# Kernel tuning notes

Measured on AMD Instinct MI355X. Metric: run time of the kernel, lower is better.

The kernel has to match this reference:

```python
import jax, jax.numpy as jnp
import numpy as np

NEG_INF = -1e9  # torch code uses masked_fill with -1e9, not -inf


def setup_inputs() -> dict:
    key = jax.random.key(0)
    ks = jax.random.split(key, 6)
    B, S, WL, D1, D2, OUT = 32, 128, 20, 300, 300, 300
    sequence = jax.random.normal(ks[0], (B, S, WL, D1), dtype=jnp.float32)
    vector = jax.random.normal(ks[1], (B, S, D2), dtype=jnp.float32)
    char_masks = jax.random.randint(ks[2], (B, S, WL), 0, 2, dtype=jnp.int32)
    W = jax.random.normal(ks[3], (OUT, D1 + D2), dtype=jnp.float32) * (1.0 / np.sqrt(D1 + D2))
    b = jax.random.normal(ks[4], (OUT,), dtype=jnp.float32) * 0.01
    v = jax.random.uniform(ks[5], (OUT,), dtype=jnp.float32, minval=-0.01, maxval=0.01)
    return {"sequence": sequence, "vector": vector, "char_masks": char_masks,
            "W": W, "b": b, "v": v}


def reference(sequence, vector, char_masks, W, b, v):
    # sequence: (B,S,WL,D1); vector: (B,S,D2); char_masks: (B,S,WL)
    D1 = sequence.shape[-1]
    # Linear on concat([sequence, vector_expanded]) == split matmul (avoids
    # materializing the (B,S,WL,D1+D2) concat):
    Ws, Wv = W[:, :D1], W[:, D1:]
    lin = (jnp.einsum('bswd,od->bswo', sequence, Ws)
           + jnp.einsum('bsd,od->bso', vector, Wv)[:, :, None, :]
           + b)                       # (B,S,WL,OUT)
    score = jnp.einsum('bswo,o->bsw', jnp.tanh(lin), v)  # (B,S,WL)
    score = jnp.where(char_masks == 0, NEG_INF, score)
    alphas = jax.nn.softmax(score, axis=2)               # over word_len
    weighted = jnp.einsum('bsw,bswd->bsd', alphas, sequence)  # (B,S,D1)
    return weighted
```

## Files before the change

kernel.cpp:

```cpp
#include <hip/hip_runtime.h>
#include <math.h>

#define NEG_INF -1000000000.0f

#define WL_  20
#define D1_  300
#define D2_  300
#define OUT_ 300
#define BS_  4096
#define PPB  4
#define NBLK (BS_ / PPB)
#define BM   80
#define KS   10
#define FR   512

typedef __attribute__((ext_vector_type(8))) short bf16x8;
typedef __attribute__((ext_vector_type(8))) short short8v;
typedef __attribute__((ext_vector_type(4))) float f32x4;
typedef __attribute__((ext_vector_type(4))) unsigned int uint4v;

__device__ short g_Bpk[KS * 20 * FR];
__device__ short g_Vpk[256 * KS * FR];
__device__ short g_Wvpk[KS * 20 * FR];
__device__ float g_vlin[(size_t)BS_ * 320];

__device__ inline short f2bf(float f) {
    unsigned u = __float_as_uint(f);
    u += 0x7FFFu + ((u >> 16) & 1u);
    return (short)(u >> 16);
}
__device__ inline float bf2f(short s) {
    return __uint_as_float(((unsigned)(unsigned short)s) << 16);
}

__device__ inline void pack_store(short* Am, int s, int lane, float4 fa, float4 fb) {
    unsigned u0 = __float_as_uint(fa.x) + 0x8000u;
    unsigned u1 = __float_as_uint(fa.y) + 0x8000u;
    unsigned u2 = __float_as_uint(fa.z) + 0x8000u;
    unsigned u3 = __float_as_uint(fa.w) + 0x8000u;
    unsigned u4 = __float_as_uint(fb.x) + 0x8000u;
    unsigned u5 = __float_as_uint(fb.y) + 0x8000u;
    unsigned u6 = __float_as_uint(fb.z) + 0x8000u;
    unsigned u7 = __float_as_uint(fb.w) + 0x8000u;
    uint4v w;
    w.x = __builtin_amdgcn_perm(u1, u0, 0x07060302u);
    w.y = __builtin_amdgcn_perm(u3, u2, 0x07060302u);
    w.z = __builtin_amdgcn_perm(u5, u4, 0x07060302u);
    w.w = __builtin_amdgcn_perm(u7, u6, 0x07060302u);
    *(uint4v*)(Am + ((size_t)s * 64 + lane) * 8) = w;
}

#define GV (256 * KS * 64)
#define GB (KS * 20 * 64)
#define GT (GV + GB + GB)

__global__ __launch_bounds__(256) void prep_small(
    const float* __restrict__ vec, const float* __restrict__ W,
    const float* __restrict__ bias,
    short* Bpk, short* Vpk, short* Wvpk)
{
    if (!Bpk) { Bpk = g_Bpk; Vpk = g_Vpk; Wvpk = g_Wvpk; }
    const int id = blockIdx.x * 256 + threadIdx.x;
    if (id >= GT) return;
    short8v o8 = {0, 0, 0, 0, 0, 0, 0, 0};
    if (id < GV) {
        const int lane = id & 63, g = id >> 6;
        const int q = lane >> 4, l15 = lane & 15;
        const int ks = g % KS, mtile = g / KS;
        const int row = mtile * 16 + l15;
        const int k0 = ks * 32 + q * 8;
        const float* s = vec + (size_t)row * D2_ + k0;
        #pragma unroll
        for (int e = 0; e < 8; ++e) {
            const int k = k0 + e;
            if (k < D2_) o8[e] = f2bf(s[e]);
            else if (k == 319) o8[e] = (short)0x3F80;
        }
        *(short8v*)(Vpk + (size_t)id * 8) = o8;
    } else if (id < GV + GB) {
        const int id3 = id - GV;
        const int lane = id3 & 63, g = id3 >> 6;
        const int q = lane >> 4, l15 = lane & 15;
        const int ks = g / 20, tile = g % 20;
        const int o = tile * 16 + l15, k0 = ks * 32 + q * 8;
        if (o < OUT_) {
            #pragma unroll
            for (int e = 0; e < 8; ++e) {
                const int k = k0 + e;
                if (k < D1_) o8[e] = f2bf(W[(size_t)o * (D1_ + D2_) + k]);
            }
        }
        *(short8v*)(Bpk + (size_t)id3 * 8) = o8;
    } else {
        const int id4 = id - GV - GB;
        const int lane = id4 & 63, g = id4 >> 6;
        const int q = lane >> 4, l15 = lane & 15;
        const int ks = g / 20, tile = g % 20;
        const int o = tile * 16 + l15, k0 = ks * 32 + q * 8;
        if (o < OUT_) {
            #pragma unroll
            for (int e = 0; e < 8; ++e) {
                const int k = k0 + e;
                if (k < D2_)        o8[e] = f2bf(W[(size_t)o * (D1_ + D2_) + D1_ + k]);
                else if (k == 319)  o8[e] = f2bf(bias[o]);
            }
        }
        *(short8v*)(Wvpk + (size_t)id4 * 8) = o8;
    }
}

__global__ __launch_bounds__(256) void vlin_kernel(
    const short* Vpk, const short* Wvpk, float* vlin)
{
    if (!vlin) { Vpk = g_Vpk; Wvpk = g_Wvpk; vlin = g_vlin; }
    const int mtile = blockIdx.x;
    const int tid  = threadIdx.x;
    const int lane = tid & 63;
    const int wv   = tid >> 6;
    const int q = lane >> 4, l15 = lane & 15;
    f32x4 acc[5];
    #pragma unroll
    for (int j = 0; j < 5; ++j) acc[j] = {0.f, 0.f, 0.f, 0.f};
    const short* pa = Vpk + (size_t)mtile * KS * FR + lane * 8;
    const short* pb = Wvpk + (size_t)(wv * 5) * FR + lane * 8;
    #pragma unroll
    for (int ks = 0; ks < KS; ++ks) {
        const bf16x8 a = *(const bf16x8*)pa; pa += FR;
        #pragma unroll
        for (int j = 0; j < 5; ++j) {
            const bf16x8 b = *(const bf16x8*)(pb + j * FR);
            acc[j] = __builtin_amdgcn_mfma_f32_16x16x32_bf16(a, b, acc[j], 0, 0, 0);
        }
        pb += 20 * FR;
    }
    const int row0 = mtile * 16 + q * 4;
    #pragma unroll
    for (int j = 0; j < 5; ++j)
        #pragma unroll
        for (int r = 0; r < 4; ++r)
            vlin[(size_t)(row0 + r) * 320 + (wv * 5 + j) * 16 + l15] = acc[j][r];
}

__global__ __launch_bounds__(256, 3) void attn_fused(
    const float* __restrict__ seq,
    const int*   __restrict__ masks,
    const float* __restrict__ vvec,
    const short* Bpk,
    const float* vlinbuf,
    float*       __restrict__ out)
{
    if (!Bpk) { Bpk = g_Bpk; vlinbuf = g_vlin; }

    __shared__ short Am[5 * KS * FR];
    __shared__ float sp[4][BM];
    __shared__ float alpha_lds[BM];

    const int tid  = threadIdx.x;
    const int lane = tid & 63;
    const int wv   = tid >> 6;
    const int q    = lane >> 4;
    const int l15  = lane & 15;
    const int blk  = blockIdx.x;

    {
        const float* sbase = seq + (size_t)blk * BM * D1_;
        float4 ra[13], rb[13];
        #pragma unroll
        for (int it = 0; it < 13; ++it) {
            const int s = wv + it * 4;
            float4 fa = {0.f, 0.f, 0.f, 0.f}, fb = {0.f, 0.f, 0.f, 0.f};
            if (s < 50) {
                const int tile = s / KS, ks = s % KS;
                const int row = tile * 16 + l15;
                const int k0 = ks * 32 + q * 8;
                const float* p = sbase + (size_t)row * D1_ + k0;
                if (k0 < 296) { fa = *(const float4*)p; fb = *(const float4*)(p + 4); }
                else if (k0 == 296) { fa = *(const float4*)p; }
            }
            ra[it] = fa; rb[it] = fb;
        }
        #pragma unroll
        for (int it = 0; it < 13; ++it) {
            const int s = wv + it * 4;
            if (s < 50) pack_store(Am, s, lane, ra[it], rb[it]);
        }
    }

    float vj[5];
    #pragma unroll
    for (int j = 0; j < 5; ++j) {
        const int col = wv * 80 + j * 16 + l15;
        vj[j] = (col < OUT_) ? vvec[col] : 0.f;
    }
    float vlp[4][5];
    #pragma unroll
    for (int p = 0; p < 4; ++p)
        #pragma unroll
        for (int j = 0; j < 5; ++j)
            vlp[p][j] = vlinbuf[(size_t)(blk * PPB + p) * 320 + wv * 80 + j * 16 + l15];
    __syncthreads();

    f32x4 acc[5][5];
    #pragma unroll
    for (int i = 0; i < 5; ++i)
        #pragma unroll
        for (int j = 0; j < 5; ++j) acc[i][j] = {0.f, 0.f, 0.f, 0.f};

    const short* pb[5];
    #pragma unroll
    for (int j = 0; j < 5; ++j)
        pb[j] = Bpk + (size_t)(wv * 5 + j) * FR + lane * 8;

    #pragma unroll
    for (int ks = 0; ks < KS; ++ks) {
        bf16x8 a[5], b[5];
        #pragma unroll
        for (int i = 0; i < 5; ++i)
            a[i] = *(const bf16x8*)(Am + (((size_t)i * KS + ks) * 64 + lane) * 8);
        #pragma unroll
        for (int j = 0; j < 5; ++j)
            b[j] = *(const bf16x8*)(pb[j] + (size_t)ks * 20 * FR);
        #pragma unroll
        for (int i = 0; i < 5; ++i)
            #pragma unroll
            for (int j = 0; j < 5; ++j)
                acc[i][j] = __builtin_amdgcn_mfma_f32_16x16x32_bf16(a[i], b[j], acc[i][j], 0, 0, 0);
    }

    #pragma unroll
    for (int i = 0; i < 5; ++i) {
        const int pLo = (16 * i) / 20;
        const int pHi = (16 * i + 15) / 20;
        #pragma unroll
        for (int r = 0; r < 4; ++r) {
            const int row = i * 16 + q * 4 + r;
            const bool hi = (row >= 20 * pHi);
            float s = 0.f;
            #pragma unroll
            for (int j = 0; j < 5; ++j) {
                const float vlv = (pLo == pHi) ? vlp[pLo][j]
                                               : (hi ? vlp[pHi][j] : vlp[pLo][j]);
                const float x = acc[i][j][r] + vlv;
                const float e = __expf(2.f * x);
                s += (1.f - 2.f / (e + 1.f)) * vj[j];
            }
            s += __shfl_xor(s, 1, 64);
            s += __shfl_xor(s, 2, 64);
            s += __shfl_xor(s, 4, 64);
            s += __shfl_xor(s, 8, 64);
            if (l15 == 0) sp[wv][row] = s;
        }
    }
    __syncthreads();

    if (tid < 128) {
        const int p = tid >> 5;
        const int w = tid & 31;
        float s;
        if (w < WL_) {
            const int row = p * WL_ + w;
            const float sc = sp[0][row] + sp[1][row] + sp[2][row] + sp[3][row];
            const int mk = masks[(size_t)(blk * PPB + p) * WL_ + w];
            s = (mk == 0) ? NEG_INF : sc;
        } else {
            s = -INFINITY;
        }
        float m = s;
        #pragma unroll
        for (int off = 16; off; off >>= 1)
            m = fmaxf(m, __shfl_xor(m, off, 32));
        const float e = __expf(s - m);
        float sum = e;
        #pragma unroll
        for (int off = 16; off; off >>= 1)
            sum += __shfl_xor(sum, off, 32);
        if (w < WL_) alpha_lds[p * WL_ + w] = e / sum;
    }
    __syncthreads();

    if (tid < PPB * 38) {
        const int p = tid / 38, ch = tid % 38;
        const int ks2 = ch >> 2, q2 = ch & 3;
        const int wst = ch % WL_;
        float o8[8] = {0.f, 0.f, 0.f, 0.f, 0.f, 0.f, 0.f, 0.f};
        #pragma unroll
        for (int wi = 0; wi < WL_; ++wi) {
            int w = wst + wi; if (w >= WL_) w -= WL_;
            const int row = p * WL_ + w;
            const int tl = row >> 4, l = row & 15;
            const bf16x8 s8 = *(const bf16x8*)(Am + (((size_t)tl * KS + ks2) * 64 + q2 * 16 + l) * 8);
            const float a = alpha_lds[row];
            #pragma unroll
            for (int e2 = 0; e2 < 8; ++e2) o8[e2] += a * bf2f(s8[e2]);
        }
        const int d0 = ch * 8, gp = blk * PPB + p;
        float* dst = out + (size_t)gp * OUT_ + d0;
        if (d0 + 8 <= OUT_) {
            *(float4*)dst       = {o8[0], o8[1], o8[2], o8[3]};
            *(float4*)(dst + 4) = {o8[4], o8[5], o8[6], o8[7]};
        } else {
            *(float4*)dst = {o8[0], o8[1], o8[2], o8[3]};
        }
    }
}

extern "C" void kernel_launch(void* const* d_in, const int* in_sizes, int n_in,
                              void* d_out, int out_size, void* d_ws, size_t ws_size,
                              hipStream_t stream) {
    const float* seq   = (const float*)d_in[0];
    const float* vec   = (const float*)d_in[1];
    const int*   masks = (const int*)d_in[2];
    const float* W     = (const float*)d_in[3];
    const float* b     = (const float*)d_in[4];
    const float* v     = (const float*)d_in[5];
    float* out = (float*)d_out;

    constexpr size_t SZ_B = sizeof(short) * (size_t)KS * 20 * FR;
    constexpr size_t SZ_V = sizeof(short) * (size_t)256 * KS * FR;
    constexpr size_t SZ_L = sizeof(float) * (size_t)BS_ * 320;
    constexpr size_t NEED = SZ_B * 2 + SZ_V + SZ_L;
    short *Bpk = nullptr, *Wvpk = nullptr, *Vpk = nullptr;
    float *vlin = nullptr;
    if (d_ws && ws_size >= NEED) {
        char* p = (char*)d_ws;
        Bpk  = (short*)p; p += SZ_B;
        Wvpk = (short*)p; p += SZ_B;
        Vpk  = (short*)p; p += SZ_V;
        vlin = (float*)p;
    }

    prep_small<<<(GT + 255) / 256, 256, 0, stream>>>(vec, W, b, Bpk, Vpk, Wvpk);
    vlin_kernel<<<256, 256, 0, stream>>>(Vpk, Wvpk, vlin);
    attn_fused<<<NBLK, 256, 0, stream>>>(seq, masks, v, Bpk, vlin, out);
}
```

Baseline: 212.0 us.

## Fuse vector projection GEMM into attention kernel, drop vlin pass

Removes the separate vlin kernel and its packed-vector buffer. Each attention block now computes the vector-side projection (plus bias) for its 4 positions with MFMA, using only 4 of 16 rows, and broadcasts the results via shuffles. This cuts one kernel launch and the global round-trip of the vlin buffer. In exchange it wastes MFMA rows, adds per-block latency before the main GEMM, and lowers the occupancy hint from 3 to 2 blocks per CU.

After: 211.0 us. No clear change (-0.5%).

```diff
diff --git a/kernel.cpp b/kernel.cpp
--- a/kernel.cpp
+++ b/kernel.cpp
@@ -20,9 +20,7 @@
 typedef __attribute__((ext_vector_type(4))) unsigned int uint4v;
 
 __device__ short g_Bpk[KS * 20 * FR];
-__device__ short g_Vpk[256 * KS * FR];
 __device__ short g_Wvpk[KS * 20 * FR];
-__device__ float g_vlin[(size_t)BS_ * 320];
 
 __device__ inline short f2bf(float f) {
     unsigned u = __float_as_uint(f);
@@ -50,36 +48,19 @@
     *(uint4v*)(Am + ((size_t)s * 64 + lane) * 8) = w;
 }
 
-#define GV (256 * KS * 64)
 #define GB (KS * 20 * 64)
-#define GT (GV + GB + GB)
+#define GT2 (GB + GB)
 
 __global__ __launch_bounds__(256) void prep_small(
-    const float* __restrict__ vec, const float* __restrict__ W,
-    const float* __restrict__ bias,
-    short* Bpk, short* Vpk, short* Wvpk)
+    const float* __restrict__ W, const float* __restrict__ bias,
+    short* Bpk, short* Wvpk)
 {
-    if (!Bpk) { Bpk = g_Bpk; Vpk = g_Vpk; Wvpk = g_Wvpk; }
+    if (!Bpk) { Bpk = g_Bpk; Wvpk = g_Wvpk; }
     const int id = blockIdx.x * 256 + threadIdx.x;
-    if (id >= GT) return;
+    if (id >= GT2) return;
     short8v o8 = {0, 0, 0, 0, 0, 0, 0, 0};
-    if (id < GV) {
+    if (id < GB) {
         const int lane = id & 63, g = id >> 6;
-        const int q = lane >> 4, l15 = lane & 15;
-        const int ks = g % KS, mtile = g / KS;
-        const int row = mtile * 16 + l15;
-        const int k0 = ks * 32 + q * 8;
-        const float* s = vec + (size_t)row * D2_ + k0;
-        #pragma unroll
-        for (int e = 0; e < 8; ++e) {
-            const int k = k0 + e;
-            if (k < D2_) o8[e] = f2bf(s[e]);
-            else if (k == 319) o8[e] = (short)0x3F80;
-        }
-        *(short8v*)(Vpk + (size_t)id * 8) = o8;
-    } else if (id < GV + GB) {
-        const int id3 = id - GV;
-        const int lane = id3 & 63, g = id3 >> 6;
         const int q = lane >> 4, l15 = lane & 15;
         const int ks = g / 20, tile = g % 20;
         const int o = tile * 16 + l15, k0 = ks * 32 + q * 8;
@@ -90,9 +71,9 @@
                 if (k < D1_) o8[e] = f2bf(W[(size_t)o * (D1_ + D2_) + k]);
             }
         }
-        *(short8v*)(Bpk + (size_t)id3 * 8) = o8;
+        *(short8v*)(Bpk + (size_t)id * 8) = o8;
     } else {
-        const int id4 = id - GV - GB;
+        const int id4 = id - GB;
         const int lane = id4 & 63, g = id4 >> 6;
         const int q = lane >> 4, l15 = lane & 15;
         const int ks = g / 20, tile = g % 20;
@@ -109,47 +90,15 @@
     }
 }
 
-__global__ __launch_bounds__(256) void vlin_kernel(
-    const short* Vpk, const short* Wvpk, float* vlin)
-{
-    if (!vlin) { Vpk = g_Vpk; Wvpk = g_Wvpk; vlin = g_vlin; }
-    const int mtile = blockIdx.x;
-    const int tid  = threadIdx.x;
-    const int lane = tid & 63;
-    const int wv   = tid >> 6;
-    const int q = lane >> 4, l15 = lane & 15;
-    f32x4 acc[5];
-    #pragma unroll
-    for (int j = 0; j < 5; ++j) acc[j] = {0.f, 0.f, 0.f, 0.f};
-    const short* pa = Vpk + (size_t)mtile * KS * FR + lane * 8;
-    const short* pb = Wvpk + (size_t)(wv * 5) * FR + lane * 8;
-    #pragma unroll
-    for (int ks = 0; ks < KS; ++ks) {
-        const bf16x8 a = *(const bf16x8*)pa; pa += FR;
-        #pragma unroll
-        for (int j = 0; j < 5; ++j) {
-            const bf16x8 b = *(const bf16x8*)(pb + j * FR);
-            acc[j] = __builtin_amdgcn_mfma_f32_16x16x32_bf16(a, b, acc[j], 0, 0, 0);
-        }
-        pb += 20 * FR;
-    }
-    const int row0 = mtile * 16 + q * 4;
-    #pragma unroll
-    for (int j = 0; j < 5; ++j)
-        #pragma unroll
-        for (int r = 0; r < 4; ++r)
-            vlin[(size_t)(row0 + r) * 320 + (wv * 5 + j) * 16 + l15] = acc[j][r];
-}
-
-__global__ __launch_bounds__(256, 3) void attn_fused(
+__global__ __launch_bounds__(256, 2) void attn_fused(
     const float* __restrict__ seq,
+    const float* __restrict__ vec,
     const int*   __restrict__ masks,
     const float* __restrict__ vvec,
-    const short* Bpk,
-    const float* vlinbuf,
+    const short* Bpk, const short* Wvpk,
     float*       __restrict__ out)
 {
-    if (!Bpk) { Bpk = g_Bpk; vlinbuf = g_vlin; }
+    if (!Bpk) { Bpk = g_Bpk; Wvpk = g_Wvpk; }
 
     __shared__ short Am[5 * KS * FR];
     __shared__ float sp[4][BM];
@@ -192,12 +141,40 @@
         const int col = wv * 80 + j * 16 + l15;
         vj[j] = (col < OUT_) ? vvec[col] : 0.f;
     }
+
+    f32x4 vacc[5];
+    #pragma unroll
+    for (int j = 0; j < 5; ++j) vacc[j] = {0.f, 0.f, 0.f, 0.f};
+    {
+        const short* pwb = Wvpk + (size_t)(wv * 5) * FR + lane * 8;
+        const float* vp = vec + (size_t)(blk * PPB + (l15 & 3)) * D2_;
+        #pragma unroll
+        for (int ks = 0; ks < KS; ++ks) {
+            const int k0 = ks * 32 + q * 8;
+            short8v av = {0, 0, 0, 0, 0, 0, 0, 0};
+            if (l15 < PPB) {
+                #pragma unroll
+                for (int e = 0; e < 8; ++e) {
+                    const int k = k0 + e;
+                    if (k < D2_)       av[e] = f2bf(vp[k]);
+                    else if (k == 319) av[e] = (short)0x3F80;
+                }
+            }
+            #pragma unroll
+            for (int j = 0; j < 5; ++j) {
+                const bf16x8 b = *(const bf16x8*)(pwb + j * FR);
+                vacc[j] = __builtin_amdgcn_mfma_f32_16x16x32_bf16(
+                    (bf16x8)av, b, vacc[j], 0, 0, 0);
+            }
+            pwb += 20 * FR;
+        }
+    }
     float vlp[4][5];
     #pragma unroll
     for (int p = 0; p < 4; ++p)
         #pragma unroll
         for (int j = 0; j < 5; ++j)
-            vlp[p][j] = vlinbuf[(size_t)(blk * PPB + p) * 320 + wv * 80 + j * 16 + l15];
+            vlp[p][j] = __shfl(vacc[j][p], l15, 64);
     __syncthreads();
 
     f32x4 acc[5][5];
@@ -316,20 +293,14 @@
     float* out = (float*)d_out;
 
     constexpr size_t SZ_B = sizeof(short) * (size_t)KS * 20 * FR;
-    constexpr size_t SZ_V = sizeof(short) * (size_t)256 * KS * FR;
-    constexpr size_t SZ_L = sizeof(float) * (size_t)BS_ * 320;
-    constexpr size_t NEED = SZ_B * 2 + SZ_V + SZ_L;
-    short *Bpk = nullptr, *Wvpk = nullptr, *Vpk = nullptr;
-    float *vlin = nullptr;
+    constexpr size_t NEED = SZ_B * 2;
+    short *Bpk = nullptr, *Wvpk = nullptr;
     if (d_ws && ws_size >= NEED) {
         char* p = (char*)d_ws;
         Bpk  = (short*)p; p += SZ_B;
-        Wvpk = (short*)p; p += SZ_B;
-        Vpk  = (short*)p; p += SZ_V;
-        vlin = (float*)p;
-    }
-
-    prep_small<<<(GT + 255) / 256, 256, 0, stream>>>(vec, W, b, Bpk, Vpk, Wvpk);
-    vlin_kernel<<<256, 256, 0, stream>>>(Vpk, Wvpk, vlin);
-    attn_fused<<<NBLK, 256, 0, stream>>>(seq, masks, v, Bpk, vlin, out);
-}
+        Wvpk = (short*)p;
+    }
+
+    prep_small<<<(GT2 + 255) / 256, 256, 0, stream>>>(W, b, Bpk, Wvpk);
+    attn_fused<<<NBLK, 256, 0, stream>>>(seq, vec, masks, v, Bpk, Wvpk, out);
+}
```
